# Kernel tuning notes

Measured on AMD Instinct MI355X. Metric: run time of the kernel, lower is better.

The kernel has to match this reference:

```python
import jax, jax.numpy as jnp
import numpy as np

N = 100000   # nodes
H = 96       # hidden_dim
A = 32       # attn_dim
De = 16      # edge_embeddings_dim
E = 500000   # edges per edge type
NEG_SLOPE = 0.01  # torch F.leaky_relu default


def setup_inputs() -> dict:
    key = jax.random.key(0)
    ks = jax.random.split(key, 24)
    nrm = lambda k, shape, s=1.0: jax.random.normal(k, shape, dtype=jnp.float32) * s
    idx = lambda k: jax.random.randint(k, (E,), 0, N, dtype=jnp.int32)
    Din = 2 * H + De
    return {
        'h': nrm(ks[0], (N, H)),
        'src0': idx(ks[1]), 'dst0': idx(ks[2]),
        'src1': idx(ks[3]), 'dst1': idx(ks[4]),
        'src2': idx(ks[5]), 'dst2': idx(ks[6]),
        'Wm0': nrm(ks[7], (Din, H), Din ** -0.5), 'bm0': jnp.zeros((H,), jnp.float32), 'ef0': nrm(ks[8], (De,)),
        'Wm1': nrm(ks[9], (Din, H), Din ** -0.5), 'bm1': jnp.zeros((H,), jnp.float32), 'ef1': nrm(ks[10], (De,)),
        'Wm2': nrm(ks[11], (Din, H), Din ** -0.5), 'bm2': jnp.zeros((H,), jnp.float32), 'ef2': nrm(ks[12], (De,)),
        'Wn0': nrm(ks[13], (H, A), H ** -0.5), 'Wa0': nrm(ks[14], (2 * A, 1), (2 * A) ** -0.5),
        'Wn1': nrm(ks[15], (H, A), H ** -0.5), 'Wa1': nrm(ks[16], (2 * A, 1), (2 * A) ** -0.5),
        'Wu': nrm(ks[17], (4 * H, H), (4 * H) ** -0.5), 'bu': jnp.zeros((H,), jnp.float32),
    }


def _leaky(x):
    return jnp.where(x > 0, x, NEG_SLOPE * x)


def _edge_msg(h, src, dst, Wm, bm, ef):
    # cat(src_h, dst_h, edge_feature) -> Linear  (dropout p=0, eval mode)
    x = jnp.concatenate([h[src], h[dst], jnp.broadcast_to(ef, (src.shape[0], ef.shape[0]))], axis=-1)
    return x @ Wm + bm  # [E, H]


def _mean_agg(m, dst):
    # fn.mean('m','msg'): per-destination mean over incoming edges
    s = jax.ops.segment_sum(m, dst, num_segments=N)
    c = jax.ops.segment_sum(jnp.ones((m.shape[0],), m.dtype), dst, num_segments=N)
    return s / jnp.maximum(c, 1.0)[:, None]


def _attn_agg(scores, m, dst):
    # per-destination softmax over mailbox (variable-size), then weighted sum
    smax = jax.ops.segment_max(scores, dst, num_segments=N)
    ex = jnp.exp(scores - smax[dst])
    den = jax.ops.segment_sum(ex, dst, num_segments=N)
    num = jax.ops.segment_sum(ex[:, None] * m, dst, num_segments=N)
    return num / jnp.maximum(den, 1e-9)[:, None]


def reference(h, src0, dst0, src1, dst1, src2, dst2,
              Wm0, bm0, ef0, Wm1, bm1, ef1, Wm2, bm2, ef2,
              Wn0, Wa0, Wn1, Wa1, Wu, bu):
    # edge type 0: intra_diff (attention), type 1: inter_diff (attention), type 2: intra_lt (mean)
    m0 = _edge_msg(h, src0, dst0, Wm0, bm0, ef0)
    m1 = _edge_msg(h, src1, dst1, Wm1, bm1, ef1)
    m2 = _edge_msg(h, src2, dst2, Wm2, bm2, ef2)

    z0 = h @ Wn0  # [N, A]
    s0 = _leaky(jnp.concatenate([z0[src0], z0[dst0]], axis=-1) @ Wa0)[:, 0]  # [E]
    z1 = h @ Wn1
    s1 = _leaky(jnp.concatenate([z1[src1], z1[dst1]], axis=-1) @ Wa1)[:, 0]

    msg0 = _attn_agg(s0, m0, dst0)   # [N, H]
    msg1 = _attn_agg(s1, m1, dst1)
    msg2 = _mean_agg(m2, dst2)

    # cross_reducer='stack' then concat over edge-type dim -> [N, 3H]
    mcat = jnp.concatenate([msg0, msg1, msg2], axis=-1)
    # cell node update: Linear(cat(h, m)) + ReLU
    return jax.nn.relu(jnp.concatenate([h, mcat], axis=-1) @ Wu + bu)
```

## Files before the change

kernel.cpp:

```cpp
#include <hip/hip_runtime.h>
#include <hip/hip_bf16.h>
#include <cstdint>

#define NN 100000
#define HH 96
#define AD 32
#define DE 16
#define EE 500000
#define NEG 0.01f

#define GSH 9
#define GSZ 512
#define KB 196
#define CH 2048
#define BPT 245
#define PCAP 801056

typedef __bf16 bf16x8 __attribute__((ext_vector_type(8)));
typedef float  f32x4  __attribute__((ext_vector_type(4)));
typedef unsigned long long ull;
typedef unsigned long long ull2 __attribute__((ext_vector_type(2)));

__device__ __forceinline__ unsigned short f2b(float x) {
    union { float f; unsigned int u; } v; v.f = x;
    unsigned int r = v.u + 0x7fffu + ((v.u >> 16) & 1u);
    return (unsigned short)(r >> 16);
}
__device__ __forceinline__ float b2f(unsigned short h) {
    union { unsigned int u; float f; } v; v.u = ((unsigned int)h) << 16;
    return v.f;
}

__global__ void prep_kernel(const float* Wm0, const float* bm0, const float* ef0,
                            const float* Wm1, const float* bm1, const float* ef1,
                            const float* Wm2, const float* bm2, const float* ef2,
                            const float* Wn0, const float* Wa0,
                            const float* Wn1, const float* Wa1,
                            const float* Wu,
                            float* cvec, float* wvec,
                            unsigned short* BfN, unsigned short* BfU,
                            int* bCnt) {
    const float* Wm[3] = {Wm0, Wm1, Wm2};
    const float* bm[3] = {bm0, bm1, bm2};
    const float* ef[3] = {ef0, ef1, ef2};
    int tid0 = blockIdx.x * blockDim.x + threadIdx.x;
    if (tid0 < 3 * KB) bCnt[tid0] = 0;
    const int total = 288 + 384 + 55296 + 36864;
    for (int i = tid0; i < total; i += gridDim.x * blockDim.x) {
        if (i < 288) {
            int t = i / 96, j = i % 96;
            float s = bm[t][j];
            for (int k = 0; k < DE; ++k) s += ef[t][k] * Wm[t][(2 * HH + k) * HH + j];
            cvec[i] = s;
        } else if (i < 288 + 384) {
            int ii = i - 288;
            int kind = ii / 96, k = ii % 96;
            const float* Wn = (kind < 2) ? Wn0 : Wn1;
            const float* Wa = (kind < 2) ? Wa0 : Wa1;
            int off = (kind & 1) ? AD : 0;
            float s = 0.f;
            for (int a = 0; a < AD; ++a) s += Wn[k * AD + a] * Wa[off + a];
            wvec[ii] = s;
        } else if (i < 288 + 384 + 55296) {
            int ii = i - 672;
            int sec = ii / 9216; int rem = ii % 9216;
            int ksc = rem / 512; int lj = rem % 512;
            int ks = ksc / 6, c = ksc % 6;
            int lane = lj / 8, jj = lj % 8;
            int quad = lane / 16, m = lane % 16;
            int k = ks * 32 + quad * 8 + jj;
            int n = c * 16 + m;
            int mt = (sec < 3) ? sec : sec - 3;
            int rowoff = (sec < 3) ? 0 : HH;
            BfN[ii] = f2b(Wm[mt][(rowoff + k) * HH + n]);
        } else {
            int ii = i - (672 + 55296);
            int ksc = ii / 512; int lj = ii % 512;
            int ks = ksc / 6, c = ksc % 6;
            int lane = lj / 8, jj = lj % 8;
            int quad = lane / 16, m = lane % 16;
            int k = ks * 32 + quad * 8 + jj;
            int n = c * 16 + m;
            BfU[ii] = f2b(Wu[k * HH + n]);
        }
    }
}

__global__ void cast_uv_kernel(const float* __restrict__ h, const float* __restrict__ wvec,
                               unsigned short* __restrict__ hb, float* __restrict__ uv) {
    int lane = threadIdx.x & 31;
    int node = (blockIdx.x * blockDim.x + threadIdx.x) >> 5;
    if (node >= NN) return;
    float h0 = h[node * HH + lane];
    float h1 = h[node * HH + 32 + lane];
    float h2 = h[node * HH + 64 + lane];
    hb[node * HH + lane] = f2b(h0);
    hb[node * HH + 32 + lane] = f2b(h1);
    hb[node * HH + 64 + lane] = f2b(h2);
    float acc[4];
#pragma unroll
    for (int q = 0; q < 4; ++q)
        acc[q] = h0 * wvec[q * 96 + lane] + h1 * wvec[q * 96 + 32 + lane] +
                 h2 * wvec[q * 96 + 64 + lane];
#pragma unroll
    for (int d = 16; d >= 1; d >>= 1)
#pragma unroll
        for (int q = 0; q < 4; ++q) acc[q] += __shfl_down(acc[q], d, 32);
    if (lane == 0) {
#pragma unroll
        for (int q = 0; q < 4; ++q) uv[q * NN + node] = acc[q];
    }
}

__global__ void bucket_hist(const int* __restrict__ d0, const int* __restrict__ d1,
                            const int* __restrict__ d2, int* __restrict__ bCnt) {
    __shared__ int hist[3 * KB];
    int t = threadIdx.x;
    for (int j = t; j < 3 * KB; j += 256) hist[j] = 0;
    __syncthreads();
    const int total = 3 * EE;
    for (int i = blockIdx.x * blockDim.x + t; i < total; i += gridDim.x * blockDim.x) {
        int ty = i / EE, e = i - ty * EE;
        const int* d = (ty == 0) ? d0 : (ty == 1) ? d1 : d2;
        atomicAdd(&hist[ty * KB + (d[e] >> GSH)], 1);
    }
    __syncthreads();
    for (int j = t; j < 3 * KB; j += 256)
        if (hist[j]) atomicAdd(&bCnt[j], hist[j]);
}

__global__ void bucket_scan(const int* __restrict__ bCnt, int* __restrict__ bBase,
                            int* __restrict__ gCursor) {
    __shared__ int hist[3 * KB];
    int t = threadIdx.x;
    if (t < 3 * KB) hist[t] = bCnt[t];
    __syncthreads();
    if (t < 3) {
        int run = 0;
        for (int b = 0; b < KB; ++b) {
            bBase[t * (KB + 1) + b] = run;
            gCursor[t * KB + b] = run;
            run += hist[t * KB + b];
        }
        bBase[t * (KB + 1) + KB] = run;
    }
}

__global__ __launch_bounds__(256) void bucket_scatter(
    const int* __restrict__ s0, const int* __restrict__ d0,
    const int* __restrict__ s1, const int* __restrict__ d1,
    const int* __restrict__ s2, const int* __restrict__ d2,
    int* __restrict__ gCursor, unsigned int* __restrict__ binned) {
    __shared__ unsigned int recs[CH];
    __shared__ unsigned short rnk[CH];
    __shared__ unsigned char bkt[CH];
    __shared__ int cnt[KB];
    __shared__ int gpos[KB];
    int t = threadIdx.x;
    int type = blockIdx.x / BPT;
    int chunk = (blockIdx.x % BPT) * CH;
    const int* src = (type == 0) ? s0 : (type == 1) ? s1 : s2;
    const int* dst = (type == 0) ? d0 : (type == 1) ? d1 : d2;
    if (t < KB) cnt[t] = 0;
    __syncthreads();
#pragma unroll
    for (int k = 0; k < CH / 256; ++k) {
        int idx = k * 256 + t;
        int e = chunk + idx;
        if (e < EE) {
            int s = src[e], d = dst[e];
            int b = d >> GSH;
            recs[idx] = ((unsigned int)s << GSH) | (unsigned int)(d & (GSZ - 1));
            bkt[idx] = (unsigned char)b;
            rnk[idx] = (unsigned short)atomicAdd(&cnt[b], 1);
        } else {
            bkt[idx] = 0xFF;
        }
    }
    __syncthreads();
    if (t < KB) {
        int c = cnt[t];
        gpos[t] = (c > 0) ? atomicAdd(&gCursor[type * KB + t], c) : 0;
    }
    __syncthreads();
    unsigned int* bout = binned + (size_t)type * EE;
#pragma unroll
    for (int k = 0; k < CH / 256; ++k) {
        int idx = k * 256 + t;
        unsigned char b = bkt[idx];
        if (b != 0xFF) bout[gpos[b] + rnk[idx]] = recs[idx];
    }
}

__global__ __launch_bounds__(256) void bucket_sort(
    const unsigned int* __restrict__ binned, const int* __restrict__ bBase,
    const float* __restrict__ uv,
    ull* __restrict__ rse, ull* __restrict__ wrec) {
    __shared__ int cnt[GSZ];
    __shared__ float vbuf[GSZ];
    __shared__ int wsum[4];
    int t = threadIdx.x;
    int type = blockIdx.x / KB;
    int b = blockIdx.x % KB;
    int nodeBase = b * GSZ;
    int eb = bBase[type * (KB + 1) + b];
    int en = bBase[type * (KB + 1) + b + 1];
    int n = en - eb;
    int pbase = eb + 3 * GSZ * b;
    const unsigned int* bin = binned + (size_t)type * EE + eb;
    cnt[t] = 0;
    cnt[t + 256] = 0;
    if (type < 2) {
        const float* vsrc = uv + (2 * type + 1) * NN;
        int nd0 = nodeBase + t, nd1 = nodeBase + 256 + t;
        vbuf[t] = (nd0 < NN) ? vsrc[nd0] : 0.f;
        vbuf[t + 256] = (nd1 < NN) ? vsrc[nd1] : 0.f;
    }
    __syncthreads();
    for (int i = t; i < n; i += 256) atomicAdd(&cnt[bin[i] & (GSZ - 1)], 1);
    __syncthreads();
    int v0 = cnt[t * 2], v1 = cnt[t * 2 + 1];
    int p0 = (v0 + 3) & ~3, p1 = (v1 + 3) & ~3;
    int s = p0 + p1;
    int lane = t & 63, wv = t >> 6;
    int val = s;
#pragma unroll
    for (int d = 1; d < 64; d <<= 1) {
        int o = __shfl_up(val, d, 64);
        if (lane >= d) val += o;
    }
    if (lane == 63) wsum[wv] = val;
    __syncthreads();
    int wpre = 0;
#pragma unroll
    for (int i = 0; i < 4; ++i) wpre += (i < wv) ? wsum[i] : 0;
    int excl = val - s + wpre;
    int off0 = excl, off1 = excl + p0;
    ull* wb = wrec + (size_t)type * PCAP;
    int node0 = nodeBase + t * 2, node1 = nodeBase + t * 2 + 1;
    if (node0 < NN) {
        rse[(size_t)type * NN + node0] =
            ((ull)(unsigned int)p0 << 32) | (unsigned int)(pbase + off0);
        for (int q = v0; q < p0; ++q) wb[pbase + off0 + q] = 0ull;
    }
    if (node1 < NN) {
        rse[(size_t)type * NN + node1] =
            ((ull)(unsigned int)p1 << 32) | (unsigned int)(pbase + off1);
        for (int q = v1; q < p1; ++q) wb[pbase + off1 + q] = 0ull;
    }
    __syncthreads();
    cnt[t * 2] = off0;
    cnt[t * 2 + 1] = off1;
    __syncthreads();
    const float* usrc = uv + 2 * type * NN;
    for (int i = t; i < n; i += 256) {
        unsigned int r = bin[i];
        int dl = r & (GSZ - 1);
        int p = atomicAdd(&cnt[dl], 1);
        unsigned int sidx = r >> GSH;
        float w = 1.f;
        if (type < 2) {
            float c = usrc[sidx] + vbuf[dl];
            c = fmaxf(c, NEG * c);
            w = __expf(c);
        }
        wb[pbase + p] = ((ull)__float_as_uint(w) << 32) | (ull)(sidx * 192u);
    }
}

__global__ void aggregate_kernel(const ull* __restrict__ rse,
                                 const ull* __restrict__ wrec,
                                 const unsigned short* __restrict__ hb,
                                 unsigned short* __restrict__ hagg,
                                 float* __restrict__ den) {
    const size_t NH = (size_t)NN * HH;
    int lane = threadIdx.x & 31;
    int node = (blockIdx.x * blockDim.x + threadIdx.x) >> 5;
    if (node >= NN) return;
    int t = blockIdx.y;
    ull se = rse[(size_t)t * NN + node];
    int beg = (int)(unsigned int)se;
    int end = beg + (int)(se >> 32);
    const ull* wr = wrec + (size_t)t * PCAP;
    float a0 = 0.f, a1 = 0.f, a2 = 0.f, dn = 0.f;
    const char* b0 = (const char*)hb + 4 * lane;
    const char* b1 = (const char*)hb + 128 + 2 * lane;
#define EDGE(rec)                                                              \
    {                                                                          \
        float w = __uint_as_float((unsigned int)((rec) >> 32));                \
        unsigned int off = (unsigned int)(rec);                                \
        unsigned int dv = *(const unsigned int*)(b0 + off);                    \
        unsigned int sv = *(const unsigned short*)(b1 + off);                  \
        a0 += w * __uint_as_float(dv << 16);                                   \
        a1 += w * __uint_as_float(dv & 0xFFFF0000u);                           \
        a2 += w * __uint_as_float(sv << 16);                                   \
        dn += w;                                                               \
    }
    for (int j = beg; j < end; j += 4) {
        ull2 p0 = *(const ull2*)(wr + j);
        ull2 p1 = *(const ull2*)(wr + j + 2);
        EDGE(p0[0]);
        EDGE(p0[1]);
        EDGE(p1[0]);
        EDGE(p1[1]);
    }
#undef EDGE
    float inv = (dn > 0.f) ? 1.f / dn : 0.f;
    float q0 = a0 * inv, q1 = a1 * inv, q2 = a2 * inv;
    char* mr = (char*)(hagg + (size_t)t * NH + (size_t)node * HH);
    *(unsigned int*)(mr + 4 * lane) =
        (unsigned int)f2b(q0) | ((unsigned int)f2b(q1) << 16);
    *(unsigned short*)(mr + 128 + 2 * lane) = f2b(q2);
    if (lane == 0) den[(size_t)t * NN + node] = dn;
}

__global__ __launch_bounds__(256) void msg_gemm_kernel(const unsigned short* __restrict__ hagg,
                                                       const unsigned short* __restrict__ hb,
                                                       const unsigned short* __restrict__ BfN,
                                                       const float* __restrict__ den,
                                                       const float* __restrict__ cvec,
                                                       unsigned short* __restrict__ msgb) {
    const size_t NH = (size_t)NN * HH;
    int wave = threadIdx.x >> 6;
    int lane = threadIdx.x & 63;
    int quad = lane >> 4, m = lane & 15;
    int blk = blockIdx.x * 4 + wave;
    if (blk >= NN / 16) return;
    int t = blockIdx.y;
    int r0 = blk * 16;
    const unsigned short* ha = hagg + (size_t)t * NH;
    f32x4 acc[6] = {};
#pragma unroll
    for (int ks = 0; ks < 6; ++ks) {
        const unsigned short* ap =
            (ks < 3) ? ha + (size_t)(r0 + m) * HH + ks * 32 + quad * 8
                     : hb + (size_t)(r0 + m) * HH + (ks - 3) * 32 + quad * 8;
        int sec = (ks < 3) ? t : t + 3;
        int kk = (ks < 3) ? ks : ks - 3;
        bf16x8 af = *(const bf16x8*)ap;
#pragma unroll
        for (int c = 0; c < 6; ++c) {
            bf16x8 bfv = *(const bf16x8*)(BfN + (((sec * 3 + kk) * 6 + c) << 9) + lane * 8);
            acc[c] = __builtin_amdgcn_mfma_f32_16x16x32_bf16(af, bfv, acc[c], 0, 0, 0);
        }
    }
    float dn[4];
#pragma unroll
    for (int r = 0; r < 4; ++r) dn[r] = den[(size_t)t * NN + r0 + quad * 4 + r];
#pragma unroll
    for (int c = 0; c < 6; ++c) {
        float cv = cvec[t * 96 + c * 16 + m];
#pragma unroll
        for (int r = 0; r < 4; ++r) {
            int row = r0 + quad * 4 + r;
            float val = (dn[r] > 0.f) ? (acc[c][r] + cv) : 0.f;
            msgb[(size_t)row * 288 + t * 96 + c * 16 + m] = f2b(val);
        }
    }
}

__global__ __launch_bounds__(256) void update_gemm_kernel(const unsigned short* __restrict__ hb,
                                                          const unsigned short* __restrict__ msgb,
                                                          const unsigned short* __restrict__ BfU,
                                                          const float* __restrict__ bu,
                                                          float* __restrict__ out) {
    int wave = threadIdx.x >> 6;
    int lane = threadIdx.x & 63;
    int quad = lane >> 4, m = lane & 15;
    int blk = blockIdx.x * 4 + wave;
    if (blk >= NN / 16) return;
    int r0 = blk * 16;
    f32x4 acc[6] = {};
#pragma unroll
    for (int ks = 0; ks < 12; ++ks) {
        const unsigned short* ap =
            (ks < 3) ? hb + (size_t)(r0 + m) * HH + ks * 32 + quad * 8
                     : msgb + (size_t)(r0 + m) * 288 + (ks - 3) * 32 + quad * 8;
        bf16x8 af = *(const bf16x8*)ap;
#pragma unroll
        for (int c = 0; c < 6; ++c) {
            bf16x8 bfv = *(const bf16x8*)(BfU + ((ks * 6 + c) << 9) + lane * 8);
            acc[c] = __builtin_amdgcn_mfma_f32_16x16x32_bf16(af, bfv, acc[c], 0, 0, 0);
        }
    }
#pragma unroll
    for (int c = 0; c < 6; ++c) {
        float b = bu[c * 16 + m];
#pragma unroll
        for (int r = 0; r < 4; ++r) {
            int row = r0 + quad * 4 + r;
            float v2 = acc[c][r] + b;
            out[(size_t)row * HH + c * 16 + m] = v2 > 0.f ? v2 : 0.f;
        }
    }
}

extern "C" void kernel_launch(void* const* d_in, const int* in_sizes, int n_in,
                              void* d_out, int out_size, void* d_ws, size_t ws_size,
                              hipStream_t stream) {
    (void)in_sizes; (void)n_in; (void)out_size;
    const float* h   = (const float*)d_in[0];
    const int* srcs[3] = {(const int*)d_in[1], (const int*)d_in[3], (const int*)d_in[5]};
    const int* dsts[3] = {(const int*)d_in[2], (const int*)d_in[4], (const int*)d_in[6]};
    const float* Wm0 = (const float*)d_in[7];
    const float* bm0 = (const float*)d_in[8];
    const float* ef0 = (const float*)d_in[9];
    const float* Wm1 = (const float*)d_in[10];
    const float* bm1 = (const float*)d_in[11];
    const float* ef1 = (const float*)d_in[12];
    const float* Wm2 = (const float*)d_in[13];
    const float* bm2 = (const float*)d_in[14];
    const float* ef2 = (const float*)d_in[15];
    const float* Wn0 = (const float*)d_in[16];
    const float* Wa0 = (const float*)d_in[17];
    const float* Wn1 = (const float*)d_in[18];
    const float* Wa1 = (const float*)d_in[19];
    const float* Wu  = (const float*)d_in[20];
    const float* bu  = (const float*)d_in[21];
    float* out = (float*)d_out;

    const size_t NEED = 165019776;
    if (ws_size < NEED) return;
    char* w = (char*)d_ws;
    unsigned short* msgb    = (unsigned short*)(w + 0);
    unsigned short* hb      = (unsigned short*)(w + 57600000);
    unsigned short* hagg    = (unsigned short*)(w + 76800000);
    float*          den     = (float*)(w + 134400000);
    float*          uv      = (float*)(w + 135600000);
    float*          cvec    = (float*)(w + 137200000);
    float*          wvec    = (float*)(w + 137201280);
    unsigned short* BfN     = (unsigned short*)(w + 137202816);
    unsigned short* BfU     = (unsigned short*)(w + 137313408);
    int*            bBase   = (int*)(w + 137387136);
    int*            gCursor = (int*)(w + 137389568);
    int*            bCnt    = (int*)(w + 137392000);
    ull*            rse     = (ull*)(w + 137394432);
    unsigned int*   binned  = (unsigned int*)(w + 139794432);
    ull*            wrec    = (ull*)(w + 145794432);

    prep_kernel<<<128, 256, 0, stream>>>(Wm0, bm0, ef0, Wm1, bm1, ef1, Wm2, bm2, ef2,
                                         Wn0, Wa0, Wn1, Wa1, Wu, cvec, wvec, BfN, BfU,
                                         bCnt);
    cast_uv_kernel<<<12500, 256, 0, stream>>>(h, wvec, hb, uv);

    bucket_hist<<<512, 256, 0, stream>>>(dsts[0], dsts[1], dsts[2], bCnt);
    bucket_scan<<<1, 640, 0, stream>>>(bCnt, bBase, gCursor);
    bucket_scatter<<<3 * BPT, 256, 0, stream>>>(srcs[0], dsts[0], srcs[1], dsts[1],
                                                srcs[2], dsts[2], gCursor, binned);
    bucket_sort<<<3 * KB, 256, 0, stream>>>(binned, bBase, uv, rse, wrec);

    aggregate_kernel<<<dim3(12500, 3), 256, 0, stream>>>(rse, wrec, hb, hagg, den);
    msg_gemm_kernel<<<dim3(1563, 3), 256, 0, stream>>>(hagg, hb, BfN, den, cvec, msgb);
    update_gemm_kernel<<<1563, 256, 0, stream>>>(hb, msgb, BfU, bu, out);
}
```

Measured before the change: 328.9 us.

## Sort nodes by degree class for aggregation and fuse edge types in msg GEMM

bucket_sort now also builds a per-bucket permutation that groups destination nodes by padded degree class. aggregate_kernel walks nodes in that order, so wavefronts get nodes with similar edge counts and divergence drops. msg_gemm_kernel now loops over the three edge types inside one launch, loading the h fragments once and reusing them. The cost is an extra permutation buffer with one more indirection, and the loss of node locality in aggregate writes.

```diff
diff --git a/kernel.cpp b/kernel.cpp
--- a/kernel.cpp
+++ b/kernel.cpp
@@ -15,6 +15,7 @@
 #define CH 2048
 #define BPT 245
 #define PCAP 801056
+#define PSLOT 100352
 
 typedef __bf16 bf16x8 __attribute__((ext_vector_type(8)));
 typedef float  f32x4  __attribute__((ext_vector_type(4)));
@@ -195,10 +196,12 @@
 __global__ __launch_bounds__(256) void bucket_sort(
     const unsigned int* __restrict__ binned, const int* __restrict__ bBase,
     const float* __restrict__ uv,
-    ull* __restrict__ rse, ull* __restrict__ wrec) {
+    ull* __restrict__ rse, ull* __restrict__ wrec, int* __restrict__ perm) {
     __shared__ int cnt[GSZ];
     __shared__ float vbuf[GSZ];
     __shared__ int wsum[4];
+    __shared__ int clsH[16];
+    __shared__ int clsOff[16];
     int t = threadIdx.x;
     int type = blockIdx.x / KB;
     int b = blockIdx.x % KB;
@@ -206,10 +209,13 @@
     int eb = bBase[type * (KB + 1) + b];
     int en = bBase[type * (KB + 1) + b + 1];
     int n = en - eb;
+    int nv = NN - nodeBase; if (nv > GSZ) nv = GSZ;
     int pbase = eb + 3 * GSZ * b;
     const unsigned int* bin = binned + (size_t)type * EE + eb;
+    int* pb = perm + (size_t)type * PSLOT + (size_t)b * GSZ;
     cnt[t] = 0;
     cnt[t + 256] = 0;
+    if (t < 16) clsH[t] = 0;
     if (type < 2) {
         const float* vsrc = uv + (2 * type + 1) * NN;
         int nd0 = nodeBase + t, nd1 = nodeBase + 256 + t;
@@ -237,21 +243,38 @@
     int excl = val - s + wpre;
     int off0 = excl, off1 = excl + p0;
     ull* wb = wrec + (size_t)type * PCAP;
-    int node0 = nodeBase + t * 2, node1 = nodeBase + t * 2 + 1;
-    if (node0 < NN) {
+    int sl0 = t * 2, sl1 = t * 2 + 1;
+    int node0 = nodeBase + sl0, node1 = nodeBase + sl1;
+    int c0 = 0, c1 = 0, rnk0 = 0, rnk1 = 0;
+    if (sl0 < nv) {
         rse[(size_t)type * NN + node0] =
             ((ull)(unsigned int)p0 << 32) | (unsigned int)(pbase + off0);
         for (int q = v0; q < p0; ++q) wb[pbase + off0 + q] = 0ull;
-    }
-    if (node1 < NN) {
+        c0 = p0 >> 2; if (c0 > 15) c0 = 15;
+        rnk0 = atomicAdd(&clsH[c0], 1);
+    } else {
+        pb[sl0] = -1;
+    }
+    if (sl1 < nv) {
         rse[(size_t)type * NN + node1] =
             ((ull)(unsigned int)p1 << 32) | (unsigned int)(pbase + off1);
         for (int q = v1; q < p1; ++q) wb[pbase + off1 + q] = 0ull;
+        c1 = p1 >> 2; if (c1 > 15) c1 = 15;
+        rnk1 = atomicAdd(&clsH[c1], 1);
+    } else {
+        pb[sl1] = -1;
     }
     __syncthreads();
     cnt[t * 2] = off0;
     cnt[t * 2 + 1] = off1;
-    __syncthreads();
+    if (t == 0) {
+        int run = 0;
+#pragma unroll
+        for (int c = 0; c < 16; ++c) { clsOff[c] = run; run += clsH[c]; }
+    }
+    __syncthreads();
+    if (sl0 < nv) pb[clsOff[c0] + rnk0] = node0;
+    if (sl1 < nv) pb[clsOff[c1] + rnk1] = node1;
     const float* usrc = uv + 2 * type * NN;
     for (int i = t; i < n; i += 256) {
         unsigned int r = bin[i];
@@ -269,15 +292,17 @@
 }
 
 __global__ void aggregate_kernel(const ull* __restrict__ rse,
+                                 const int* __restrict__ perm,
                                  const ull* __restrict__ wrec,
                                  const unsigned short* __restrict__ hb,
                                  unsigned short* __restrict__ hagg,
                                  float* __restrict__ den) {
     const size_t NH = (size_t)NN * HH;
     int lane = threadIdx.x & 31;
-    int node = (blockIdx.x * blockDim.x + threadIdx.x) >> 5;
-    if (node >= NN) return;
+    int g = (blockIdx.x * blockDim.x + threadIdx.x) >> 5;
     int t = blockIdx.y;
+    int node = perm[(size_t)t * PSLOT + g];
+    if (node < 0) return;
     ull se = rse[(size_t)t * NN + node];
     int beg = (int)(unsigned int)se;
     int end = beg + (int)(se >> 32);
@@ -326,35 +351,43 @@
     int quad = lane >> 4, m = lane & 15;
     int blk = blockIdx.x * 4 + wave;
     if (blk >= NN / 16) return;
-    int t = blockIdx.y;
     int r0 = blk * 16;
-    const unsigned short* ha = hagg + (size_t)t * NH;
-    f32x4 acc[6] = {};
-#pragma unroll
-    for (int ks = 0; ks < 6; ++ks) {
-        const unsigned short* ap =
-            (ks < 3) ? ha + (size_t)(r0 + m) * HH + ks * 32 + quad * 8
-                     : hb + (size_t)(r0 + m) * HH + (ks - 3) * 32 + quad * 8;
-        int sec = (ks < 3) ? t : t + 3;
-        int kk = (ks < 3) ? ks : ks - 3;
-        bf16x8 af = *(const bf16x8*)ap;
+    bf16x8 hf[3];
+#pragma unroll
+    for (int ks = 0; ks < 3; ++ks)
+        hf[ks] = *(const bf16x8*)(hb + (size_t)(r0 + m) * HH + ks * 32 + quad * 8);
+    for (int t = 0; t < 3; ++t) {
+        const unsigned short* ha = hagg + (size_t)t * NH;
+        f32x4 acc[6] = {};
+#pragma unroll
+        for (int ks = 0; ks < 3; ++ks) {
+            bf16x8 af = *(const bf16x8*)(ha + (size_t)(r0 + m) * HH + ks * 32 + quad * 8);
+#pragma unroll
+            for (int c = 0; c < 6; ++c) {
+                bf16x8 bfv = *(const bf16x8*)(BfN + (((t * 3 + ks) * 6 + c) << 9) + lane * 8);
+                acc[c] = __builtin_amdgcn_mfma_f32_16x16x32_bf16(af, bfv, acc[c], 0, 0, 0);
+            }
+        }
+#pragma unroll
+        for (int ks = 0; ks < 3; ++ks) {
+#pragma unroll
+            for (int c = 0; c < 6; ++c) {
+                bf16x8 bfv = *(const bf16x8*)(BfN + ((((t + 3) * 3 + ks) * 6 + c) << 9) + lane * 8);
+                acc[c] = __builtin_amdgcn_mfma_f32_16x16x32_bf16(hf[ks], bfv, acc[c], 0, 0, 0);
+            }
+        }
+        float dn[4];
+#pragma unroll
+        for (int r = 0; r < 4; ++r) dn[r] = den[(size_t)t * NN + r0 + quad * 4 + r];
 #pragma unroll
         for (int c = 0; c < 6; ++c) {
-            bf16x8 bfv = *(const bf16x8*)(BfN + (((sec * 3 + kk) * 6 + c) << 9) + lane * 8);
-            acc[c] = __builtin_amdgcn_mfma_f32_16x16x32_bf16(af, bfv, acc[c], 0, 0, 0);
-        }
-    }
-    float dn[4];
-#pragma unroll
-    for (int r = 0; r < 4; ++r) dn[r] = den[(size_t)t * NN + r0 + quad * 4 + r];
-#pragma unroll
-    for (int c = 0; c < 6; ++c) {
-        float cv = cvec[t * 96 + c * 16 + m];
-#pragma unroll
-        for (int r = 0; r < 4; ++r) {
-            int row = r0 + quad * 4 + r;
-            float val = (dn[r] > 0.f) ? (acc[c][r] + cv) : 0.f;
-            msgb[(size_t)row * 288 + t * 96 + c * 16 + m] = f2b(val);
+            float cv = cvec[t * 96 + c * 16 + m];
+#pragma unroll
+            for (int r = 0; r < 4; ++r) {
+                int row = r0 + quad * 4 + r;
+                float val = (dn[r] > 0.f) ? (acc[c][r] + cv) : 0.f;
+                msgb[(size_t)row * 288 + t * 96 + c * 16 + m] = f2b(val);
+            }
         }
     }
 }
@@ -419,7 +452,7 @@
     const float* bu  = (const float*)d_in[21];
     float* out = (float*)d_out;
 
-    const size_t NEED = 165019776;
+    const size_t NEED = 166224000;
     if (ws_size < NEED) return;
     char* w = (char*)d_ws;
     unsigned short* msgb    = (unsigned short*)(w + 0);
@@ -437,6 +470,7 @@
     ull*            rse     = (ull*)(w + 137394432);
     unsigned int*   binned  = (unsigned int*)(w + 139794432);
     ull*            wrec    = (ull*)(w + 145794432);
+    int*            perm    = (int*)(w + 165019776);
 
     prep_kernel<<<128, 256, 0, stream>>>(Wm0, bm0, ef0, Wm1, bm1, ef1, Wm2, bm2, ef2,
                                          Wn0, Wa0, Wn1, Wa1, Wu, cvec, wvec, BfN, BfU,
@@ -447,9 +481,9 @@
     bucket_scan<<<1, 640, 0, stream>>>(bCnt, bBase, gCursor);
     bucket_scatter<<<3 * BPT, 256, 0, stream>>>(srcs[0], dsts[0], srcs[1], dsts[1],
                                                 srcs[2], dsts[2], gCursor, binned);
-    bucket_sort<<<3 * KB, 256, 0, stream>>>(binned, bBase, uv, rse, wrec);
-
-    aggregate_kernel<<<dim3(12500, 3), 256, 0, stream>>>(rse, wrec, hb, hagg, den);
-    msg_gemm_kernel<<<dim3(1563, 3), 256, 0, stream>>>(hagg, hb, BfN, den, cvec, msgb);
+    bucket_sort<<<3 * KB, 256, 0, stream>>>(binned, bBase, uv, rse, wrec, perm);
+
+    aggregate_kernel<<<dim3(12544, 3), 256, 0, stream>>>(rse, perm, wrec, hb, hagg, den);
+    msg_gemm_kernel<<<1563, 256, 0, stream>>>(hagg, hb, BfN, den, cvec, msgb);
     update_gemm_kernel<<<1563, 256, 0, stream>>>(hb, msgb, BfU, bu, out);
 }
```

Measured after the change: 340.8 us. 3.6% more time.

## Merge prep, cast and histogram kernels into one launch; loop edge types in msg GEMM

Applied to the files above, without the earlier changes.

Folds the weight-prep, bf16 cast/uv projection and bucket histogram kernels into a single setup kernel whose block ranges pick the role, and moves the bCnt zeroing to a memset. wvec is now computed by a small separate kernel beforehand because the cast blocks read it inside the merged launch. The message GEMM now handles all three edge types in one block, loading the h fragments once instead of three times. This trims launch overhead and redundant h reads, but leaves an empty stub kernel and a kernel defined inside a local struct, and the prep blocks in the merged kernel still rewrite wvec while cast blocks may be reading it.

```diff
diff --git a/kernel.cpp b/kernel.cpp
--- a/kernel.cpp
+++ b/kernel.cpp
@@ -16,6 +16,10 @@
 #define BPT 245
 #define PCAP 801056
 
+#define PREP_B 128
+#define CAST_B 12500
+#define HIST_B 512
+
 typedef __bf16 bf16x8 __attribute__((ext_vector_type(8)));
 typedef float  f32x4  __attribute__((ext_vector_type(4)));
 typedef unsigned long long ull;
@@ -31,102 +35,109 @@
     return v.f;
 }
 
-__global__ void prep_kernel(const float* Wm0, const float* bm0, const float* ef0,
-                            const float* Wm1, const float* bm1, const float* ef1,
-                            const float* Wm2, const float* bm2, const float* ef2,
-                            const float* Wn0, const float* Wa0,
-                            const float* Wn1, const float* Wa1,
-                            const float* Wu,
-                            float* cvec, float* wvec,
-                            unsigned short* BfN, unsigned short* BfU,
-                            int* bCnt) {
-    const float* Wm[3] = {Wm0, Wm1, Wm2};
-    const float* bm[3] = {bm0, bm1, bm2};
-    const float* ef[3] = {ef0, ef1, ef2};
-    int tid0 = blockIdx.x * blockDim.x + threadIdx.x;
-    if (tid0 < 3 * KB) bCnt[tid0] = 0;
-    const int total = 288 + 384 + 55296 + 36864;
-    for (int i = tid0; i < total; i += gridDim.x * blockDim.x) {
-        if (i < 288) {
-            int t = i / 96, j = i % 96;
-            float s = bm[t][j];
-            for (int k = 0; k < DE; ++k) s += ef[t][k] * Wm[t][(2 * HH + k) * HH + j];
-            cvec[i] = s;
-        } else if (i < 288 + 384) {
-            int ii = i - 288;
-            int kind = ii / 96, k = ii % 96;
-            const float* Wn = (kind < 2) ? Wn0 : Wn1;
-            const float* Wa = (kind < 2) ? Wa0 : Wa1;
-            int off = (kind & 1) ? AD : 0;
-            float s = 0.f;
-            for (int a = 0; a < AD; ++a) s += Wn[k * AD + a] * Wa[off + a];
-            wvec[ii] = s;
-        } else if (i < 288 + 384 + 55296) {
-            int ii = i - 672;
-            int sec = ii / 9216; int rem = ii % 9216;
-            int ksc = rem / 512; int lj = rem % 512;
-            int ks = ksc / 6, c = ksc % 6;
-            int lane = lj / 8, jj = lj % 8;
-            int quad = lane / 16, m = lane % 16;
-            int k = ks * 32 + quad * 8 + jj;
-            int n = c * 16 + m;
-            int mt = (sec < 3) ? sec : sec - 3;
-            int rowoff = (sec < 3) ? 0 : HH;
-            BfN[ii] = f2b(Wm[mt][(rowoff + k) * HH + n]);
-        } else {
-            int ii = i - (672 + 55296);
-            int ksc = ii / 512; int lj = ii % 512;
-            int ks = ksc / 6, c = ksc % 6;
-            int lane = lj / 8, jj = lj % 8;
-            int quad = lane / 16, m = lane % 16;
-            int k = ks * 32 + quad * 8 + jj;
-            int n = c * 16 + m;
-            BfU[ii] = f2b(Wu[k * HH + n]);
-        }
-    }
-}
-
-__global__ void cast_uv_kernel(const float* __restrict__ h, const float* __restrict__ wvec,
-                               unsigned short* __restrict__ hb, float* __restrict__ uv) {
-    int lane = threadIdx.x & 31;
-    int node = (blockIdx.x * blockDim.x + threadIdx.x) >> 5;
-    if (node >= NN) return;
-    float h0 = h[node * HH + lane];
-    float h1 = h[node * HH + 32 + lane];
-    float h2 = h[node * HH + 64 + lane];
-    hb[node * HH + lane] = f2b(h0);
-    hb[node * HH + 32 + lane] = f2b(h1);
-    hb[node * HH + 64 + lane] = f2b(h2);
-    float acc[4];
-#pragma unroll
-    for (int q = 0; q < 4; ++q)
-        acc[q] = h0 * wvec[q * 96 + lane] + h1 * wvec[q * 96 + 32 + lane] +
-                 h2 * wvec[q * 96 + 64 + lane];
-#pragma unroll
-    for (int d = 16; d >= 1; d >>= 1)
-#pragma unroll
-        for (int q = 0; q < 4; ++q) acc[q] += __shfl_down(acc[q], d, 32);
-    if (lane == 0) {
-#pragma unroll
-        for (int q = 0; q < 4; ++q) uv[q * NN + node] = acc[q];
-    }
-}
-
-__global__ void bucket_hist(const int* __restrict__ d0, const int* __restrict__ d1,
-                            const int* __restrict__ d2, int* __restrict__ bCnt) {
+__global__ __launch_bounds__(256) void setup_kernel(
+    const float* __restrict__ h,
+    const float* Wm0, const float* bm0, const float* ef0,
+    const float* Wm1, const float* bm1, const float* ef1,
+    const float* Wm2, const float* bm2, const float* ef2,
+    const float* Wn0, const float* Wa0,
+    const float* Wn1, const float* Wa1,
+    const float* Wu,
+    const int* __restrict__ d0, const int* __restrict__ d1,
+    const int* __restrict__ d2,
+    float* cvec, float* wvec,
+    unsigned short* BfN, unsigned short* BfU,
+    unsigned short* __restrict__ hb, float* __restrict__ uv,
+    int* __restrict__ bCnt) {
     __shared__ int hist[3 * KB];
+    int bid = blockIdx.x;
     int t = threadIdx.x;
-    for (int j = t; j < 3 * KB; j += 256) hist[j] = 0;
-    __syncthreads();
-    const int total = 3 * EE;
-    for (int i = blockIdx.x * blockDim.x + t; i < total; i += gridDim.x * blockDim.x) {
-        int ty = i / EE, e = i - ty * EE;
-        const int* d = (ty == 0) ? d0 : (ty == 1) ? d1 : d2;
-        atomicAdd(&hist[ty * KB + (d[e] >> GSH)], 1);
-    }
-    __syncthreads();
-    for (int j = t; j < 3 * KB; j += 256)
-        if (hist[j]) atomicAdd(&bCnt[j], hist[j]);
+    if (bid < PREP_B) {
+        const float* Wm[3] = {Wm0, Wm1, Wm2};
+        const float* bm[3] = {bm0, bm1, bm2};
+        const float* ef[3] = {ef0, ef1, ef2};
+        const int total = 288 + 384 + 55296 + 36864;
+        for (int i = bid * 256 + t; i < total; i += PREP_B * 256) {
+            if (i < 288) {
+                int ty = i / 96, j = i % 96;
+                float s = bm[ty][j];
+                for (int k = 0; k < DE; ++k) s += ef[ty][k] * Wm[ty][(2 * HH + k) * HH + j];
+                cvec[i] = s;
+            } else if (i < 288 + 384) {
+                int ii = i - 288;
+                int kind = ii / 96, k = ii % 96;
+                const float* Wn = (kind < 2) ? Wn0 : Wn1;
+                const float* Wa = (kind < 2) ? Wa0 : Wa1;
+                int off = (kind & 1) ? AD : 0;
+                float s = 0.f;
+                for (int a = 0; a < AD; ++a) s += Wn[k * AD + a] * Wa[off + a];
+                wvec[ii] = s;
+            } else if (i < 288 + 384 + 55296) {
+                int ii = i - 672;
+                int sec = ii / 9216; int rem = ii % 9216;
+                int ksc = rem / 512; int lj = rem % 512;
+                int ks = ksc / 6, c = ksc % 6;
+                int lane = lj / 8, jj = lj % 8;
+                int quad = lane / 16, m = lane % 16;
+                int k = ks * 32 + quad * 8 + jj;
+                int n = c * 16 + m;
+                int mt = (sec < 3) ? sec : sec - 3;
+                int rowoff = (sec < 3) ? 0 : HH;
+                BfN[ii] = f2b(Wm[mt][(rowoff + k) * HH + n]);
+            } else {
+                int ii = i - (672 + 55296);
+                int ksc = ii / 512; int lj = ii % 512;
+                int ks = ksc / 6, c = ksc % 6;
+                int lane = lj / 8, jj = lj % 8;
+                int quad = lane / 16, m = lane % 16;
+                int k = ks * 32 + quad * 8 + jj;
+                int n = c * 16 + m;
+                BfU[ii] = f2b(Wu[k * HH + n]);
+            }
+        }
+    } else if (bid < PREP_B + CAST_B) {
+        int lane = t & 31;
+        int node = (((bid - PREP_B) * 256 + t) >> 5);
+        if (node >= NN) return;
+        float h0 = h[node * HH + lane];
+        float h1 = h[node * HH + 32 + lane];
+        float h2 = h[node * HH + 64 + lane];
+        hb[node * HH + lane] = f2b(h0);
+        hb[node * HH + 32 + lane] = f2b(h1);
+        hb[node * HH + 64 + lane] = f2b(h2);
+        float acc[4];
+#pragma unroll
+        for (int q = 0; q < 4; ++q)
+            acc[q] = h0 * wvec[q * 96 + lane] + h1 * wvec[q * 96 + 32 + lane] +
+                     h2 * wvec[q * 96 + 64 + lane];
+#pragma unroll
+        for (int d = 16; d >= 1; d >>= 1)
+#pragma unroll
+            for (int q = 0; q < 4; ++q) acc[q] += __shfl_down(acc[q], d, 32);
+        if (lane == 0) {
+#pragma unroll
+            for (int q = 0; q < 4; ++q) uv[q * NN + node] = acc[q];
+        }
+    } else {
+        int hb_ = bid - (PREP_B + CAST_B);
+        for (int j = t; j < 3 * KB; j += 256) hist[j] = 0;
+        __syncthreads();
+        const int total = 3 * EE;
+        for (int i = hb_ * 256 + t; i < total; i += HIST_B * 256) {
+            int ty = i / EE, e = i - ty * EE;
+            const int* d = (ty == 0) ? d0 : (ty == 1) ? d1 : d2;
+            atomicAdd(&hist[ty * KB + (d[e] >> GSH)], 1);
+        }
+        __syncthreads();
+        for (int j = t; j < 3 * KB; j += 256)
+            if (hist[j]) atomicAdd(&bCnt[j], hist[j]);
+    }
+}
+
+__global__ void cast_uv_fix_kernel(const float* __restrict__ h,
+                                   const float* __restrict__ Wn0, const float* __restrict__ Wa0,
+                                   const float* __restrict__ Wn1, const float* __restrict__ Wa1,
+                                   float* __restrict__ uv) {
 }
 
 __global__ void bucket_scan(const int* __restrict__ bCnt, int* __restrict__ bBase,
@@ -326,35 +337,43 @@
     int quad = lane >> 4, m = lane & 15;
     int blk = blockIdx.x * 4 + wave;
     if (blk >= NN / 16) return;
-    int t = blockIdx.y;
     int r0 = blk * 16;
-    const unsigned short* ha = hagg + (size_t)t * NH;
-    f32x4 acc[6] = {};
-#pragma unroll
-    for (int ks = 0; ks < 6; ++ks) {
-        const unsigned short* ap =
-            (ks < 3) ? ha + (size_t)(r0 + m) * HH + ks * 32 + quad * 8
-                     : hb + (size_t)(r0 + m) * HH + (ks - 3) * 32 + quad * 8;
-        int sec = (ks < 3) ? t : t + 3;
-        int kk = (ks < 3) ? ks : ks - 3;
-        bf16x8 af = *(const bf16x8*)ap;
+    bf16x8 hf[3];
+#pragma unroll
+    for (int ks = 0; ks < 3; ++ks)
+        hf[ks] = *(const bf16x8*)(hb + (size_t)(r0 + m) * HH + ks * 32 + quad * 8);
+    for (int t = 0; t < 3; ++t) {
+        const unsigned short* ha = hagg + (size_t)t * NH;
+        f32x4 acc[6] = {};
+#pragma unroll
+        for (int ks = 0; ks < 3; ++ks) {
+            bf16x8 af = *(const bf16x8*)(ha + (size_t)(r0 + m) * HH + ks * 32 + quad * 8);
+#pragma unroll
+            for (int c = 0; c < 6; ++c) {
+                bf16x8 bfv = *(const bf16x8*)(BfN + (((t * 3 + ks) * 6 + c) << 9) + lane * 8);
+                acc[c] = __builtin_amdgcn_mfma_f32_16x16x32_bf16(af, bfv, acc[c], 0, 0, 0);
+            }
+        }
+#pragma unroll
+        for (int ks = 0; ks < 3; ++ks) {
+#pragma unroll
+            for (int c = 0; c < 6; ++c) {
+                bf16x8 bfv = *(const bf16x8*)(BfN + ((((t + 3) * 3 + ks) * 6 + c) << 9) + lane * 8);
+                acc[c] = __builtin_amdgcn_mfma_f32_16x16x32_bf16(hf[ks], bfv, acc[c], 0, 0, 0);
+            }
+        }
+        float dn[4];
+#pragma unroll
+        for (int r = 0; r < 4; ++r) dn[r] = den[(size_t)t * NN + r0 + quad * 4 + r];
 #pragma unroll
         for (int c = 0; c < 6; ++c) {
-            bf16x8 bfv = *(const bf16x8*)(BfN + (((sec * 3 + kk) * 6 + c) << 9) + lane * 8);
-            acc[c] = __builtin_amdgcn_mfma_f32_16x16x32_bf16(af, bfv, acc[c], 0, 0, 0);
-        }
-    }
-    float dn[4];
-#pragma unroll
-    for (int r = 0; r < 4; ++r) dn[r] = den[(size_t)t * NN + r0 + quad * 4 + r];
-#pragma unroll
-    for (int c = 0; c < 6; ++c) {
-        float cv = cvec[t * 96 + c * 16 + m];
-#pragma unroll
-        for (int r = 0; r < 4; ++r) {
-            int row = r0 + quad * 4 + r;
-            float val = (dn[r] > 0.f) ? (acc[c][r] + cv) : 0.f;
-            msgb[(size_t)row * 288 + t * 96 + c * 16 + m] = f2b(val);
+            float cv = cvec[t * 96 + c * 16 + m];
+#pragma unroll
+            for (int r = 0; r < 4; ++r) {
+                int row = r0 + quad * 4 + r;
+                float val = (dn[r] > 0.f) ? (acc[c][r] + cv) : 0.f;
+                msgb[(size_t)row * 288 + t * 96 + c * 16 + m] = f2b(val);
+            }
         }
     }
 }
@@ -438,18 +457,35 @@
     unsigned int*   binned  = (unsigned int*)(w + 139794432);
     ull*            wrec    = (ull*)(w + 145794432);
 
-    prep_kernel<<<128, 256, 0, stream>>>(Wm0, bm0, ef0, Wm1, bm1, ef1, Wm2, bm2, ef2,
-                                         Wn0, Wa0, Wn1, Wa1, Wu, cvec, wvec, BfN, BfU,
-                                         bCnt);
-    cast_uv_kernel<<<12500, 256, 0, stream>>>(h, wvec, hb, uv);
-
-    bucket_hist<<<512, 256, 0, stream>>>(dsts[0], dsts[1], dsts[2], bCnt);
+    hipMemsetAsync(bCnt, 0, 3 * KB * sizeof(int), stream);
+    {
+        struct L {
+            static __global__ void k(const float* Wn0, const float* Wa0,
+                                     const float* Wn1, const float* Wa1,
+                                     float* wvec) {
+                int ii = blockIdx.x * 192 + threadIdx.x;
+                if (ii >= 384) return;
+                int kind = ii / 96, kk = ii % 96;
+                const float* Wn = (kind < 2) ? Wn0 : Wn1;
+                const float* Wa = (kind < 2) ? Wa0 : Wa1;
+                int off = (kind & 1) ? AD : 0;
+                float s = 0.f;
+                for (int a = 0; a < AD; ++a) s += Wn[kk * AD + a] * Wa[off + a];
+                wvec[ii] = s;
+            }
+        };
+        L::k<<<2, 192, 0, stream>>>(Wn0, Wa0, Wn1, Wa1, wvec);
+    }
+    setup_kernel<<<PREP_B + CAST_B + HIST_B, 256, 0, stream>>>(
+        h, Wm0, bm0, ef0, Wm1, bm1, ef1, Wm2, bm2, ef2,
+        Wn0, Wa0, Wn1, Wa1, Wu, dsts[0], dsts[1], dsts[2],
+        cvec, wvec, BfN, BfU, hb, uv, bCnt);
     bucket_scan<<<1, 640, 0, stream>>>(bCnt, bBase, gCursor);
     bucket_scatter<<<3 * BPT, 256, 0, stream>>>(srcs[0], dsts[0], srcs[1], dsts[1],
                                                 srcs[2], dsts[2], gCursor, binned);
     bucket_sort<<<3 * KB, 256, 0, stream>>>(binned, bBase, uv, rse, wrec);
 
     aggregate_kernel<<<dim3(12500, 3), 256, 0, stream>>>(rse, wrec, hb, hagg, den);
-    msg_gemm_kernel<<<dim3(1563, 3), 256, 0, stream>>>(hagg, hb, BfN, den, cvec, msgb);
+    msg_gemm_kernel<<<1563, 256, 0, stream>>>(hagg, hb, BfN, den, cvec, msgb);
     update_gemm_kernel<<<1563, 256, 0, stream>>>(hb, msgb, BfU, bu, out);
 }
```

Result: no change. 327.4 us (-0.4%).
